# Kernel optimization log

Hardware: AMD Instinct MI355X
Metric: run time of the kernel (lower is better)

## Reference

```python
import jax, jax.numpy as jnp
import numpy as np

BS, LATENT, HID, MAXLEN = 128, 512, 1024, 512

def setup_inputs() -> dict:
    key = jax.random.key(0)
    ks = jax.random.split(key, 12)
    s = 1.0 / np.sqrt(HID)  # pytorch default LSTM init scale
    inp = {}
    inp["decoder_input"] = jax.random.normal(ks[0], (BS, LATENT), jnp.float32)
    inp["lengths"] = jax.random.randint(ks[1], (BS,), 0, MAXLEN)
    # bidirectional single-layer LSTM params (gate order i,f,g,o; combined bias = b_ih+b_hh)
    inp["Wih_f"] = jax.random.uniform(ks[2], (4 * HID, LATENT), jnp.float32, -s, s)
    inp["Whh_f"] = jax.random.uniform(ks[3], (4 * HID, HID), jnp.float32, -s, s)
    inp["b_f"] = jax.random.uniform(ks[4], (4 * HID,), jnp.float32, -s, s)
    inp["Wih_b"] = jax.random.uniform(ks[5], (4 * HID, LATENT), jnp.float32, -s, s)
    inp["Whh_b"] = jax.random.uniform(ks[6], (4 * HID, HID), jnp.float32, -s, s)
    inp["b_b"] = jax.random.uniform(ks[7], (4 * HID,), jnp.float32, -s, s)
    # out: Linear(hidden -> latent); fc1: Linear(2*hidden -> 1)
    inp["W_out"] = jax.random.uniform(ks[8], (LATENT, HID), jnp.float32, -s, s)
    inp["b_out"] = jax.random.uniform(ks[9], (LATENT,), jnp.float32, -s, s)
    inp["W_fc1"] = jax.random.uniform(ks[10], (1, 2 * HID), jnp.float32, -s, s)
    inp["b_fc1"] = jax.random.uniform(ks[11], (1,), jnp.float32, -s, s)
    return inp

def _lstm_cell(x, h, c, Wih, Whh, b):
    z = x @ Wih.T + h @ Whh.T + b  # (bs, 4H)
    i, f, g, o = jnp.split(z, 4, axis=-1)
    c2 = jax.nn.sigmoid(f) * c + jax.nn.sigmoid(i) * jnp.tanh(g)
    h2 = jax.nn.sigmoid(o) * jnp.tanh(c2)
    return h2, c2

def reference(decoder_input, lengths, Wih_f, Whh_f, b_f, Wih_b, Whh_b, b_b,
              W_out, b_out, W_fc1, b_fc1):
    max_len = int(jnp.max(lengths))  # static decode length
    bs = decoder_input.shape[0]
    h0 = jnp.zeros((bs, HID), decoder_input.dtype)

    def step(carry, _):
        x, hf, cf, hb, cb = carry
        # bidirectional LSTM over a length-1 sequence = two cells on same input
        hf, cf = _lstm_cell(x, hf, cf, Wih_f, Whh_f, b_f)
        hb, cb = _lstm_cell(x, hb, cb, Wih_b, Whh_b, b_b)
        out_t = jnp.concatenate([hf, hb], axis=-1)  # (bs, 2H)
        # next input = out(h_n[-1]) i.e. backward-direction hidden
        x_next = hb @ W_out.T + b_out
        return (x_next, hf, cf, hb, cb), out_t

    carry0 = (decoder_input, h0, h0, h0, h0)
    _, outs = jax.lax.scan(step, carry0, xs=None, length=max_len)  # (T, bs, 2H)
    x = jnp.transpose(outs, (1, 0, 2))  # (bs, T, 2H)
    x = jax.nn.relu(x)
    return x @ W_fc1.T + b_fc1  # (bs, T, 1)
```

## Files before the change

### kernel.cpp

```cpp
#include <hip/hip_runtime.h>
#include <math.h>

typedef unsigned short u16;
typedef __attribute__((ext_vector_type(8))) short short8;
typedef __attribute__((ext_vector_type(4))) float f32x4;

__device__ __forceinline__ float sigm(float x) { return 1.0f / (1.0f + expf(-x)); }

__device__ __forceinline__ u16 f2bf(float x) {
    union { float f; unsigned u; } v; v.f = x;
    unsigned r = v.u + 0x7fffu + ((v.u >> 16) & 1u);
    return (u16)(r >> 16);
}
__device__ __forceinline__ float bf2f(u16 h) {
    union { unsigned u; float f; } v; v.u = ((unsigned)h) << 16;
    return v.f;
}
__device__ __forceinline__ f32x4 mfma16(short8 a, short8 b, f32x4 c) {
    return __builtin_amdgcn_mfma_f32_16x16x32_bf16(a, b, c, 0, 0, 0);
}
__device__ __forceinline__ void gl_lds16(const void* g, void* l) {
    __builtin_amdgcn_global_load_lds(
        (const __attribute__((address_space(1))) unsigned int*)g,
        (__attribute__((address_space(3))) unsigned int*)l, 16, 0, 0);
}
__device__ __forceinline__ int swz(int c) { return (c ^ (c >> 2)) & 3; }

#define STAGE_W(kk, buf)                                                      \
    do {                                                                      \
        _Pragma("unroll") for (int i_ = 0; i_ < 2; ++i_)                      \
            gl_lds16(Wsrc + soff[i_] + (kk),                                  \
                     sm + (buf) * 8192 + sldsoff[i_]);                        \
    } while (0)

#define LOAD_A(kk, AH_, AL_)                                                  \
    do {                                                                      \
        _Pragma("unroll") for (int ks_ = 0; ks_ < 2; ++ks_) {                 \
            AH_[ks_] = *(const short8*)(Ah + aoff + (kk) + ks_ * 32);         \
            AL_[ks_] = *(const short8*)(Al + aoff + (kk) + ks_ * 32);         \
        }                                                                     \
    } while (0)

#define COMPUTE(buf, AH_, AL_, cix)                                           \
    do {                                                                      \
        const char* bb_ = sm + (buf) * 8192;                                  \
        _Pragma("unroll") for (int ks_ = 0; ks_ < 2; ++ks_) {                 \
            short8 bh_[2], bl_[2];                                            \
            _Pragma("unroll") for (int nt_ = 0; nt_ < 2; ++nt_) {             \
                const int col_ = nt_ * 16 + l15;                              \
                const int off_ = ks_ * 2048 + col_ * 64 + ((quad ^ swz(col_)) * 16); \
                bh_[nt_] = *(const short8*)(bb_ + off_);                      \
                bl_[nt_] = *(const short8*)(bb_ + 4096 + off_);               \
            }                                                                 \
            _Pragma("unroll") for (int nt_ = 0; nt_ < 2; ++nt_) {             \
                acc[nt_] = mfma16(AH_[ks_], bh_[nt_], acc[nt_]);              \
                acc[nt_] = mfma16(AL_[ks_], bh_[nt_], acc[nt_]);              \
                acc[nt_] = mfma16(AH_[ks_], bl_[nt_], acc[nt_]);              \
            }                                                                 \
        }                                                                     \
        if (fc1w) {                                                           \
            const int kb_ = (cix) * 64 + quad * 8;                            \
            _Pragma("unroll") for (int ks_ = 0; ks_ < 2; ++ks_) {             \
                const float* wp_ = Wfc1 + kb_ + ks_ * 32;                     \
                const f32x4 w0_ = *(const f32x4*)(wp_);                       \
                const f32x4 w1_ = *(const f32x4*)(wp_ + 4);                   \
                const short8 hv_ = AH_[ks_];                                  \
                const short8 lv_ = AL_[ks_];                                  \
                _Pragma("unroll") for (int e_ = 0; e_ < 8; ++e_) {            \
                    const float v_ = bf2f((u16)hv_[e_]) + bf2f((u16)lv_[e_]); \
                    const float wv_ = (e_ < 4) ? w0_[e_] : w1_[e_ - 4];       \
                    fsum = fmaf(fmaxf(v_, 0.0f), wv_, fsum);                  \
                }                                                             \
            }                                                                 \
        }                                                                     \
    } while (0)

__global__ __launch_bounds__(256, 2) void k_step(
    const u16* __restrict__ Ah, const u16* __restrict__ Al,
    u16* __restrict__ NAh, u16* __restrict__ NAl,
    const u16* __restrict__ WH, const u16* __restrict__ WL, int wstride,
    int koff_f, int nch_f, int koff_b, int nch_b,
    const float* __restrict__ BR, float* __restrict__ CF, float* __restrict__ CB,
    const float* __restrict__ Wfc1, const float* __restrict__ bfc1,
    float* __restrict__ out, int T, int t)
{
    __shared__ __align__(16) char sm[16384];

    const int tid = threadIdx.x, bid = blockIdx.x;
    const int w = tid >> 6, lane = tid & 63, l15 = lane & 15, quad = lane >> 4;
    const int dir = bid & 1;
    const int rest = bid >> 1;
    const int rowhalf = rest >> 7, colgrp = rest & 127;
    const int nbase = dir * 4096 + colgrp * 32;
    const int koff = dir ? koff_b : koff_f;
    const int nch  = dir ? nch_b : nch_f;
    const int r0 = rowhalf * 64 + w * 16;

    const bool fc1w = (t > 0) && (dir == 0) && (colgrp == 0);

    const int sp = w >> 1, skh = w & 1;
    const u16* Wsrc = sp ? WL : WH;
    size_t soff[2];
    int sldsoff[2];
#pragma unroll
    for (int i = 0; i < 2; ++i) {
        const int col = i * 16 + (lane >> 2);
        const int s = (lane & 3) ^ swz(col);
        soff[i] = (size_t)(nbase + col) * wstride + (size_t)(koff + skh * 32 + s * 8);
        sldsoff[i] = sp * 4096 + skh * 2048 + i * 1024;
    }

    const size_t aoff = (size_t)(r0 + l15) * 2048 + (size_t)(koff + quad * 8);

    f32x4 acc[2] = {};
    short8 ahA[2], alA[2], ahB[2], alB[2];
    float fsum = 0.0f;

    STAGE_W(0, 0);
    LOAD_A(0, ahA, alA);

    for (int c = 0; c < nch; c += 2) {
        __syncthreads();
        {
            const int k1 = (c + 1) * 64;
            STAGE_W(k1, 1);
            LOAD_A(k1, ahB, alB);
        }
        COMPUTE(0, ahA, alA, c);
        __syncthreads();
        if (c + 2 < nch) {
            const int k2 = (c + 2) * 64;
            STAGE_W(k2, 0);
            LOAD_A(k2, ahA, alA);
        }
        COMPUTE(1, ahB, alB, c + 1);
    }

    __syncthreads();

    if (fc1w) {
        float v = fsum;
        v += __shfl_xor(v, 16);
        v += __shfl_xor(v, 32);
        if (lane < 16) {
            const int m = r0 + l15;
            out[(size_t)m * T + (t - 1)] = v + bfc1[0];
        }
    }

    char* zb = sm + w * 2304;
#pragma unroll
    for (int nt = 0; nt < 2; ++nt)
#pragma unroll
        for (int r = 0; r < 4; ++r)
            *(float*)(zb + (quad * 4 + r) * 144 + (nt * 16 + l15) * 4) = acc[nt][r];
    __syncthreads();

    float* C = dir ? CB : CF;
#pragma unroll
    for (int p2 = 0; p2 < 2; ++p2) {
        const int idx = p2 * 64 + lane;
        const int ml = idx >> 3;
        const int ul = idx & 7;
        const f32x4 z = *(const f32x4*)(zb + ml * 144 + ul * 16);
        const f32x4 b4 = *(const f32x4*)(BR + nbase + ul * 4);
        const float zi = z[0] + b4[0], zf = z[1] + b4[1];
        const float zg = z[2] + b4[2], zo = z[3] + b4[3];
        const int u = colgrp * 8 + ul;
        const int m = r0 + ml;
        const size_t cidx = (size_t)m * 1024 + u;
        const float cold = C[cidx];
        const float c2 = sigm(zf) * cold + sigm(zi) * tanhf(zg);
        const float h2 = sigm(zo) * tanhf(c2);
        C[cidx] = c2;
        const size_t hidx = (size_t)m * 2048 + dir * 1024 + u;
        const u16 hh = f2bf(h2);
        NAh[hidx] = hh;
        NAl[hidx] = f2bf(h2 - bf2f(hh));
    }
}

__global__ __launch_bounds__(256) void k_tail(
    const u16* __restrict__ Ah, const u16* __restrict__ Al,
    const float* __restrict__ Wfc1, const float* __restrict__ bfc1,
    float* __restrict__ out, int T)
{
    __shared__ float red[256];
    const int m = blockIdx.x, tid = threadIdx.x;
    const size_t base = (size_t)m * 2048 + tid * 8;
    const short8 hv = *(const short8*)(Ah + base);
    const short8 lv = *(const short8*)(Al + base);
    float s = 0.0f;
#pragma unroll
    for (int e = 0; e < 8; ++e) {
        const float v = bf2f((u16)hv[e]) + bf2f((u16)lv[e]);
        s = fmaf(fmaxf(v, 0.0f), Wfc1[tid * 8 + e], s);
    }
    red[tid] = s;
    __syncthreads();
    for (int off = 128; off > 0; off >>= 1) {
        if (tid < off) red[tid] += red[tid + off];
        __syncthreads();
    }
    if (tid == 0) out[(size_t)m * T + T - 1] = red[0] + bfc1[0];
}

__global__ __launch_bounds__(256, 1) void k_fold(
    const u16* __restrict__ AH, const u16* __restrict__ AL,
    const u16* __restrict__ BH, const u16* __restrict__ BL,
    const float* __restrict__ Whh_b,
    u16* __restrict__ WH, u16* __restrict__ WL)
{
    const int tid = threadIdx.x, bid = blockIdx.x;
    const int w = tid >> 6, lane = tid & 63, l15 = lane & 15, quad = lane >> 4;
    const int bm = bid >> 4, bn = bid & 15;
    const int ar0 = bm * 64 + (w & 1) * 32;
    const int br0 = bn * 64 + (w >> 1) * 32;
    f32x4 acc[2][2] = {};
    for (int k0 = 0; k0 < 512; k0 += 32) {
        short8 a_h[2], a_l[2], b_h[2], b_l[2];
#pragma unroll
        for (int mt = 0; mt < 2; ++mt) {
            const size_t o = (size_t)(ar0 + mt * 16 + l15) * 512 + k0 + quad * 8;
            a_h[mt] = *(const short8*)(AH + o);
            a_l[mt] = *(const short8*)(AL + o);
        }
#pragma unroll
        for (int nt = 0; nt < 2; ++nt) {
            const size_t o = (size_t)(br0 + nt * 16 + l15) * 512 + k0 + quad * 8;
            b_h[nt] = *(const short8*)(BH + o);
            b_l[nt] = *(const short8*)(BL + o);
        }
#pragma unroll
        for (int mt = 0; mt < 2; ++mt)
#pragma unroll
            for (int nt = 0; nt < 2; ++nt) {
                acc[mt][nt] = mfma16(a_h[mt], b_h[nt], acc[mt][nt]);
                acc[mt][nt] = mfma16(a_l[mt], b_h[nt], acc[mt][nt]);
                acc[mt][nt] = mfma16(a_h[mt], b_l[nt], acc[mt][nt]);
            }
    }
#pragma unroll
    for (int mt = 0; mt < 2; ++mt)
#pragma unroll
        for (int nt = 0; nt < 2; ++nt)
#pragma unroll
            for (int r = 0; r < 4; ++r) {
                const int row = ar0 + mt * 16 + quad * 4 + r;
                const int j = br0 + nt * 16 + l15;
                float v = acc[mt][nt][r];
                if (row >= 4096)
                    v += Whh_b[(size_t)((row & 3) * 1024 + ((row & 4095) >> 2)) * 1024 + j];
                const size_t d = (size_t)row * 2048 + 1024 + j;
                const u16 hh = f2bf(v);
                WH[d] = hh;
                WL[d] = f2bf(v - bf2f(hh));
            }
}

__global__ __launch_bounds__(256) void k_prep(
    const float* __restrict__ dec,
    const float* __restrict__ Wih_f, const float* __restrict__ Whh_f,
    const float* __restrict__ b_f, const float* __restrict__ Wih_b,
    const float* __restrict__ b_b, const float* __restrict__ W_out,
    const float* __restrict__ b_out, const float* __restrict__ b_fc1,
    u16* __restrict__ WihH, u16* __restrict__ WihL,
    u16* __restrict__ WoTH, u16* __restrict__ WoTL,
    float* __restrict__ BR0, float* __restrict__ BR1,
    u16* __restrict__ A0h, u16* __restrict__ A0l,
    u16* __restrict__ WH, u16* __restrict__ WL,
    float* __restrict__ out, int out_size)
{
    const int t = blockIdx.x * 256 + threadIdx.x;
    if (t < 524288) {
        const int colp = t >> 6, kb = (t & 63) * 8;
        const int dir = colp >> 12, u = (colp & 4095) >> 2, g = colp & 3;
        const float* src = (dir ? Wih_b : Wih_f) + (size_t)(g * 1024 + u) * 512 + kb;
        const size_t d = (size_t)colp * 512 + kb;
#pragma unroll
        for (int j = 0; j < 8; ++j) {
            const float v = src[j];
            const u16 hh = f2bf(v);
            WihH[d + j] = hh; WihL[d + j] = f2bf(v - bf2f(hh));
        }
    } else if (t < 589824) {
        const int i = t - 524288, jc = i >> 6, lb = (i & 63) * 8;
#pragma unroll
        for (int jj = 0; jj < 8; ++jj) {
            const float v = W_out[(size_t)(lb + jj) * 1024 + jc];
            const size_t d = (size_t)jc * 512 + lb + jj;
            const u16 hh = f2bf(v);
            WoTH[d] = hh; WoTL[d] = f2bf(v - bf2f(hh));
        }
    } else if (t < 598016) {
        const int colp = t - 589824;
        const int dir = colp >> 12, u = (colp & 4095) >> 2, g = colp & 3;
        const float* Wih = dir ? Wih_b : Wih_f;
        const float s = (dir ? b_b : b_f)[g * 1024 + u];
        BR0[colp] = s;
        float dot = 0.0f;
        for (int l = 0; l < 512; ++l)
            dot += Wih[(size_t)(g * 1024 + u) * 512 + l] * b_out[l];
        BR1[colp] = s + dot;
    } else if (t < 606208) {
        const int i = t - 598016, m = i >> 6, kb = (i & 63) * 8;
#pragma unroll
        for (int j = 0; j < 8; ++j) {
            const float v = dec[(size_t)m * 512 + kb + j];
            const size_t d = (size_t)m * 2048 + kb + j;
            const u16 hh = f2bf(v);
            A0h[d] = hh; A0l[d] = f2bf(v - bf2f(hh));
        }
    } else if (t < 614400) {
        const int base = (t - 606208) * 8;
        const float b0 = b_fc1[0];
#pragma unroll
        for (int j = 0; j < 8; ++j)
            if (base + j < out_size) out[base + j] = b0;
    } else {
        const int i = t - 614400, colp = i >> 7, kb = (i & 127) * 8;
        const int u = colp >> 2, g = colp & 3;
        const float* src = Whh_f + (size_t)(g * 1024 + u) * 1024 + kb;
        const size_t d = (size_t)colp * 2048 + kb;
#pragma unroll
        for (int j = 0; j < 8; ++j) {
            const float v = src[j];
            const u16 hh = f2bf(v);
            WH[d + j] = hh; WL[d + j] = f2bf(v - bf2f(hh));
        }
    }
}

extern "C" void kernel_launch(void* const* d_in, const int* in_sizes, int n_in,
                              void* d_out, int out_size, void* d_ws, size_t ws_size,
                              hipStream_t stream) {
    const float* dec   = (const float*)d_in[0];
    const float* Wih_f = (const float*)d_in[2];
    const float* Whh_f = (const float*)d_in[3];
    const float* b_f   = (const float*)d_in[4];
    const float* Wih_b = (const float*)d_in[5];
    const float* Whh_b = (const float*)d_in[6];
    const float* b_b   = (const float*)d_in[7];
    const float* W_out = (const float*)d_in[8];
    const float* b_out = (const float*)d_in[9];
    const float* W_fc1 = (const float*)d_in[10];
    const float* b_fc1 = (const float*)d_in[11];
    float* out = (float*)d_out;

    char* ws = (char*)d_ws;
    u16* WH    = (u16*)(ws);
    u16* WL    = (u16*)(ws + 33554432);
    u16* WihH  = (u16*)(ws + 67108864);
    u16* WihL  = (u16*)(ws + 75497472);
    u16* WoTH  = (u16*)(ws + 83886080);
    u16* WoTL  = (u16*)(ws + 84934656);
    u16* A0h   = (u16*)(ws + 85983232);
    u16* A0l   = (u16*)(ws + 86507520);
    u16* A1h   = (u16*)(ws + 87031808);
    u16* A1l   = (u16*)(ws + 87556096);
    float* CF  = (float*)(ws + 88080384);
    float* CB  = (float*)(ws + 88604672);
    float* BR0 = (float*)(ws + 89128960);
    float* BR1 = (float*)(ws + 89161728);

    k_prep<<<4448, 256, 0, stream>>>(dec, Wih_f, Whh_f, b_f, Wih_b, b_b,
                                     W_out, b_out, b_fc1,
                                     WihH, WihL, WoTH, WoTL, BR0, BR1,
                                     A0h, A0l, WH, WL, out, out_size);
    k_fold<<<2048, 256, 0, stream>>>(WihH, WihL, WoTH, WoTL, Whh_b, WH, WL);
    hipMemsetAsync(CF, 0, 1048576, stream);

    const int T = out_size / 128;
    u16* Abh[2] = {A0h, A1h};
    u16* Abl[2] = {A0l, A1l};
    for (int t = 0; t < T; ++t) {
        const int in = t & 1, nx = in ^ 1;
        if (t == 0) {
            k_step<<<512, 256, 0, stream>>>(A0h, A0l, A1h, A1l,
                                            WihH, WihL, 512, 0, 8, 0, 8,
                                            BR0, CF, CB, W_fc1, b_fc1, out, T, 0);
        } else {
            k_step<<<512, 256, 0, stream>>>(Abh[in], Abl[in], Abh[nx], Abl[nx],
                                            WH, WL, 2048, 0, 32, 1024, 16,
                                            BR1, CF, CB, W_fc1, b_fc1, out, T, t);
        }
    }
    k_tail<<<128, 256, 0, stream>>>(Abh[T & 1], Abl[T & 1], W_fc1, b_fc1, out, T);
}
```

Measured before the change: 21.80 ms.

## Fuse all LSTM timesteps into one persistent kernel with grid barrier

Replaces the per-timestep k_step launches with a single persistent kernel, k_steps, that loops over all timesteps and synchronises blocks through an atomic-counter grid barrier. Cell state is kept in registers instead of being round-tripped through global CF/CB buffers. The first weight chunk for the next step is prefetched into LDS before the barrier. This removes launch overhead and per-step global traffic, but it depends on all 512 blocks being co-resident (2 per CU on 256 CUs); otherwise the barrier can deadlock, and the spin-wait adds cost of its own.

Result: slower. 43.11 ms (+97.8%).

```diff
diff --git a/kernel.cpp b/kernel.cpp
--- a/kernel.cpp
+++ b/kernel.cpp
@@ -26,11 +26,30 @@
 }
 __device__ __forceinline__ int swz(int c) { return (c ^ (c >> 2)) & 3; }
 
-#define STAGE_W(kk, buf)                                                      \
+__device__ __forceinline__ void grid_barrier(unsigned* cnt, unsigned* gen,
+                                             unsigned nb, unsigned inst) {
+    __syncthreads();
+    if (threadIdx.x == 0) {
+        __threadfence();
+        const unsigned a = __hip_atomic_fetch_add(cnt, 1u, __ATOMIC_ACQ_REL,
+                                                  __HIP_MEMORY_SCOPE_AGENT);
+        if (a == nb * (inst + 1u) - 1u) {
+            __hip_atomic_store(gen, inst + 1u, __ATOMIC_RELEASE,
+                               __HIP_MEMORY_SCOPE_AGENT);
+        } else {
+            while (__hip_atomic_load(gen, __ATOMIC_RELAXED,
+                                     __HIP_MEMORY_SCOPE_AGENT) < inst + 1u)
+                __builtin_amdgcn_s_sleep(2);
+        }
+        __threadfence();
+    }
+    __syncthreads();
+}
+
+#define STAGE2(src, oa, ob, kk, buf)                                          \
     do {                                                                      \
-        _Pragma("unroll") for (int i_ = 0; i_ < 2; ++i_)                      \
-            gl_lds16(Wsrc + soff[i_] + (kk),                                  \
-                     sm + (buf) * 8192 + sldsoff[i_]);                        \
+        gl_lds16((src) + (oa) + (kk), sm + (buf) * 8192 + lds0);              \
+        gl_lds16((src) + (ob) + (kk), sm + (buf) * 8192 + lds1);              \
     } while (0)
 
 #define LOAD_A(kk, AH_, AL_)                                                  \
@@ -75,16 +94,17 @@
         }                                                                     \
     } while (0)
 
-__global__ __launch_bounds__(256, 2) void k_step(
-    const u16* __restrict__ Ah, const u16* __restrict__ Al,
-    u16* __restrict__ NAh, u16* __restrict__ NAl,
-    const u16* __restrict__ WH, const u16* __restrict__ WL, int wstride,
-    int koff_f, int nch_f, int koff_b, int nch_b,
-    const float* __restrict__ BR, float* __restrict__ CF, float* __restrict__ CB,
+__global__ __launch_bounds__(256, 2) void k_steps(
+    u16* A0h, u16* A0l, u16* A1h, u16* A1l,
+    const u16* __restrict__ WihH, const u16* __restrict__ WihL,
+    const u16* __restrict__ WH, const u16* __restrict__ WL,
+    const float* __restrict__ BR0, const float* __restrict__ BR1,
     const float* __restrict__ Wfc1, const float* __restrict__ bfc1,
-    float* __restrict__ out, int T, int t)
+    float* __restrict__ out,
+    unsigned* barcnt, unsigned* bargen, int T)
 {
     __shared__ __align__(16) char sm[16384];
+    __shared__ __align__(16) char ze[9216];
 
     const int tid = threadIdx.x, bid = blockIdx.x;
     const int w = tid >> 6, lane = tid & 63, l15 = lane & 15, quad = lane >> 4;
@@ -92,91 +112,115 @@
     const int rest = bid >> 1;
     const int rowhalf = rest >> 7, colgrp = rest & 127;
     const int nbase = dir * 4096 + colgrp * 32;
-    const int koff = dir ? koff_b : koff_f;
-    const int nch  = dir ? nch_b : nch_f;
     const int r0 = rowhalf * 64 + w * 16;
-
-    const bool fc1w = (t > 0) && (dir == 0) && (colgrp == 0);
+    const bool fc1b = (dir == 0) && (colgrp == 0);
 
     const int sp = w >> 1, skh = w & 1;
-    const u16* Wsrc = sp ? WL : WH;
-    size_t soff[2];
-    int sldsoff[2];
-#pragma unroll
-    for (int i = 0; i < 2; ++i) {
-        const int col = i * 16 + (lane >> 2);
-        const int s = (lane & 3) ^ swz(col);
-        soff[i] = (size_t)(nbase + col) * wstride + (size_t)(koff + skh * 32 + s * 8);
-        sldsoff[i] = sp * 4096 + skh * 2048 + i * 1024;
-    }
-
-    const size_t aoff = (size_t)(r0 + l15) * 2048 + (size_t)(koff + quad * 8);
-
-    f32x4 acc[2] = {};
-    short8 ahA[2], alA[2], ahB[2], alB[2];
-    float fsum = 0.0f;
-
-    STAGE_W(0, 0);
-    LOAD_A(0, ahA, alA);
-
-    for (int c = 0; c < nch; c += 2) {
-        __syncthreads();
-        {
-            const int k1 = (c + 1) * 64;
-            STAGE_W(k1, 1);
-            LOAD_A(k1, ahB, alB);
-        }
-        COMPUTE(0, ahA, alA, c);
-        __syncthreads();
-        if (c + 2 < nch) {
-            const int k2 = (c + 2) * 64;
-            STAGE_W(k2, 0);
-            LOAD_A(k2, ahA, alA);
-        }
-        COMPUTE(1, ahB, alB, c + 1);
-    }
-
-    __syncthreads();
-
-    if (fc1w) {
-        float v = fsum;
-        v += __shfl_xor(v, 16);
-        v += __shfl_xor(v, 32);
-        if (lane < 16) {
-            const int m = r0 + l15;
-            out[(size_t)m * T + (t - 1)] = v + bfc1[0];
-        }
-    }
-
-    char* zb = sm + w * 2304;
-#pragma unroll
-    for (int nt = 0; nt < 2; ++nt)
-#pragma unroll
-        for (int r = 0; r < 4; ++r)
-            *(float*)(zb + (quad * 4 + r) * 144 + (nt * 16 + l15) * 4) = acc[nt][r];
-    __syncthreads();
-
-    float* C = dir ? CB : CF;
-#pragma unroll
-    for (int p2 = 0; p2 < 2; ++p2) {
-        const int idx = p2 * 64 + lane;
-        const int ml = idx >> 3;
-        const int ul = idx & 7;
-        const f32x4 z = *(const f32x4*)(zb + ml * 144 + ul * 16);
-        const f32x4 b4 = *(const f32x4*)(BR + nbase + ul * 4);
-        const float zi = z[0] + b4[0], zf = z[1] + b4[1];
-        const float zg = z[2] + b4[2], zo = z[3] + b4[3];
-        const int u = colgrp * 8 + ul;
-        const int m = r0 + ml;
-        const size_t cidx = (size_t)m * 1024 + u;
-        const float cold = C[cidx];
-        const float c2 = sigm(zf) * cold + sigm(zi) * tanhf(zg);
-        const float h2 = sigm(zo) * tanhf(c2);
-        C[cidx] = c2;
-        const size_t hidx = (size_t)m * 2048 + dir * 1024 + u;
-        const u16 hh = f2bf(h2);
-        NAh[hidx] = hh;
-        NAl[hidx] = f2bf(h2 - bf2f(hh));
+    const u16* Wsrc0 = sp ? WihL : WihH;
+    const u16* WsrcN = sp ? WL : WH;
+    size_t s0a, s0b, sNa, sNb;
+    int lds0, lds1;
+    {
+        const int colA = 0 * 16 + (lane >> 2);
+        const int colB = 1 * 16 + (lane >> 2);
+        const int sa = (lane & 3) ^ swz(colA);
+        const int sb = (lane & 3) ^ swz(colB);
+        const size_t koffN = dir ? 1024 : 0;
+        s0a = (size_t)(nbase + colA) * 512 + (size_t)(skh * 32 + sa * 8);
+        s0b = (size_t)(nbase + colB) * 512 + (size_t)(skh * 32 + sb * 8);
+        sNa = (size_t)(nbase + colA) * 2048 + koffN + (size_t)(skh * 32 + sa * 8);
+        sNb = (size_t)(nbase + colB) * 2048 + koffN + (size_t)(skh * 32 + sb * 8);
+        lds0 = sp * 4096 + skh * 2048;
+        lds1 = lds0 + 1024;
+    }
+
+    const size_t abase = (size_t)(r0 + l15) * 2048 + (size_t)(quad * 8);
+    const size_t aoffN = abase + (size_t)(dir ? 1024 : 0);
+
+    const int ul = lane & 7;
+    const f32x4 br0v = *(const f32x4*)(BR0 + nbase + ul * 4);
+    const f32x4 br1v = *(const f32x4*)(BR1 + nbase + ul * 4);
+    const float b1 = bfc1[0];
+    float creg0 = 0.0f, creg1 = 0.0f;
+
+    const unsigned nb = gridDim.x;
+
+    STAGE2(Wsrc0, s0a, s0b, 0, 0);
+
+    for (int t = 0; t < T; ++t) {
+        const int first = (t == 0);
+        const u16* Ah = (t & 1) ? A1h : A0h;
+        const u16* Al = (t & 1) ? A1l : A0l;
+        u16* NAh = (t & 1) ? A0h : A1h;
+        u16* NAl = (t & 1) ? A0l : A1l;
+        const int nch = first ? 8 : (dir ? 16 : 32);
+        const u16* Wsrc = first ? Wsrc0 : WsrcN;
+        const size_t sA = first ? s0a : sNa;
+        const size_t sB = first ? s0b : sNb;
+        const size_t aoff = first ? abase : aoffN;
+        const bool fc1w = fc1b && (t > 0);
+
+        f32x4 acc[2] = {};
+        short8 ahA[2], alA[2], ahB[2], alB[2];
+        float fsum = 0.0f;
+
+        LOAD_A(0, ahA, alA);
+
+        for (int c = 0; c < nch; c += 2) {
+            __syncthreads();
+            {
+                const int k1 = (c + 1) * 64;
+                STAGE2(Wsrc, sA, sB, k1, 1);
+                LOAD_A(k1, ahB, alB);
+            }
+            COMPUTE(0, ahA, alA, c);
+            __syncthreads();
+            if (c + 2 < nch) {
+                const int k2 = (c + 2) * 64;
+                STAGE2(Wsrc, sA, sB, k2, 0);
+                LOAD_A(k2, ahA, alA);
+            }
+            COMPUTE(1, ahB, alB, c + 1);
+        }
+
+        if (fc1w) {
+            float v = fsum;
+            v += __shfl_xor(v, 16);
+            v += __shfl_xor(v, 32);
+            if (lane < 16)
+                out[(size_t)(r0 + l15) * T + (t - 1)] = v + b1;
+        }
+
+        char* zb = ze + w * 2304;
+#pragma unroll
+        for (int nt = 0; nt < 2; ++nt)
+#pragma unroll
+            for (int r = 0; r < 4; ++r)
+                *(float*)(zb + (quad * 4 + r) * 144 + (nt * 16 + l15) * 4) = acc[nt][r];
+
+        if (t + 1 < T) STAGE2(WsrcN, sNa, sNb, 0, 0);
+
+        const f32x4 bv = first ? br0v : br1v;
+#pragma unroll
+        for (int p2 = 0; p2 < 2; ++p2) {
+            const int ml = p2 * 8 + (lane >> 3);
+            const f32x4 z = *(const f32x4*)(zb + ml * 144 + ul * 16);
+            const float zi = z[0] + bv[0], zf = z[1] + bv[1];
+            const float zg = z[2] + bv[2], zo = z[3] + bv[3];
+            const float cold = p2 ? creg1 : creg0;
+            const float c2 = sigm(zf) * cold + sigm(zi) * tanhf(zg);
+            const float h2 = sigm(zo) * tanhf(c2);
+            if (p2) creg1 = c2; else creg0 = c2;
+            const int u = colgrp * 8 + ul;
+            const int m = r0 + ml;
+            const size_t hidx = (size_t)m * 2048 + dir * 1024 + u;
+            const u16 hh = f2bf(h2);
+            NAh[hidx] = hh;
+            NAl[hidx] = f2bf(h2 - bf2f(hh));
+        }
+
+        if (t + 1 < T)
+            grid_barrier(barcnt, bargen, nb, (unsigned)t);
     }
 }
 
@@ -358,32 +402,23 @@
     u16* A0l   = (u16*)(ws + 86507520);
     u16* A1h   = (u16*)(ws + 87031808);
     u16* A1l   = (u16*)(ws + 87556096);
-    float* CF  = (float*)(ws + 88080384);
-    float* CB  = (float*)(ws + 88604672);
     float* BR0 = (float*)(ws + 89128960);
     float* BR1 = (float*)(ws + 89161728);
+    unsigned* barcnt = (unsigned*)(ws + 89194496);
+    unsigned* bargen = (unsigned*)(ws + 89194624);
 
     k_prep<<<4448, 256, 0, stream>>>(dec, Wih_f, Whh_f, b_f, Wih_b, b_b,
                                      W_out, b_out, b_fc1,
                                      WihH, WihL, WoTH, WoTL, BR0, BR1,
                                      A0h, A0l, WH, WL, out, out_size);
     k_fold<<<2048, 256, 0, stream>>>(WihH, WihL, WoTH, WoTL, Whh_b, WH, WL);
-    hipMemsetAsync(CF, 0, 1048576, stream);
+    hipMemsetAsync(ws + 89194496, 0, 256, stream);
 
     const int T = out_size / 128;
-    u16* Abh[2] = {A0h, A1h};
-    u16* Abl[2] = {A0l, A1l};
-    for (int t = 0; t < T; ++t) {
-        const int in = t & 1, nx = in ^ 1;
-        if (t == 0) {
-            k_step<<<512, 256, 0, stream>>>(A0h, A0l, A1h, A1l,
-                                            WihH, WihL, 512, 0, 8, 0, 8,
-                                            BR0, CF, CB, W_fc1, b_fc1, out, T, 0);
-        } else {
-            k_step<<<512, 256, 0, stream>>>(Abh[in], Abl[in], Abh[nx], Abl[nx],
-                                            WH, WL, 2048, 0, 32, 1024, 16,
-                                            BR1, CF, CB, W_fc1, b_fc1, out, T, t);
-        }
-    }
-    k_tail<<<128, 256, 0, stream>>>(Abh[T & 1], Abl[T & 1], W_fc1, b_fc1, out, T);
-}
+    k_steps<<<512, 256, 0, stream>>>(A0h, A0l, A1h, A1l,
+                                     WihH, WihL, WH, WL,
+                                     BR0, BR1, W_fc1, b_fc1, out,
+                                     barcnt, bargen, T);
+    k_tail<<<128, 256, 0, stream>>>((T & 1) ? A1h : A0h, (T & 1) ? A1l : A0l,
+                                    W_fc1, b_fc1, out, T);
+}
```

## Deepen weight staging to four LDS buffers with vmcnt-gated single barriers

Applied to the files above, without the earlier changes.

Replaces the two-buffer, two-__syncthreads-per-pair loop with a four-stage ring. Each chunk uses one s_barrier, gated by s_waitcnt vmcnt(16), and prefetches both the weight tiles and the A fragments three chunks ahead. The fc1 weights are copied into LDS once, and the gate-staging epilogue gets its own LDS buffer, which removes one block-wide barrier. The goal is to hide global/LDS load latency in the latency-bound per-timestep GEMM. The cost is more LDS and registers, plus a prefetch that runs past the final chunk.

New measurement: 20.79 ms. 4.6% less time.

```diff
diff --git a/kernel.cpp b/kernel.cpp
--- a/kernel.cpp
+++ b/kernel.cpp
@@ -26,11 +26,12 @@
 }
 __device__ __forceinline__ int swz(int c) { return (c ^ (c >> 2)) & 3; }
 
+#define FENCE() asm volatile("" ::: "memory")
+
 #define STAGE_W(kk, buf)                                                      \
     do {                                                                      \
-        _Pragma("unroll") for (int i_ = 0; i_ < 2; ++i_)                      \
-            gl_lds16(Wsrc + soff[i_] + (kk),                                  \
-                     sm + (buf) * 8192 + sldsoff[i_]);                        \
+        gl_lds16(Wsrc + sA + (kk), sm + (buf) * 8192 + lds0);                 \
+        gl_lds16(Wsrc + sB + (kk), sm + (buf) * 8192 + lds1);                 \
     } while (0)
 
 #define LOAD_A(kk, AH_, AL_)                                                  \
@@ -41,9 +42,9 @@
         }                                                                     \
     } while (0)
 
-#define COMPUTE(buf, AH_, AL_, cix)                                           \
+#define COMPUTE(bix, AH_, AL_, cix)                                           \
     do {                                                                      \
-        const char* bb_ = sm + (buf) * 8192;                                  \
+        const char* bb_ = sm + (bix) * 8192;                                  \
         _Pragma("unroll") for (int ks_ = 0; ks_ < 2; ++ks_) {                 \
             short8 bh_[2], bl_[2];                                            \
             _Pragma("unroll") for (int nt_ = 0; nt_ < 2; ++nt_) {             \
@@ -61,7 +62,7 @@
         if (fc1w) {                                                           \
             const int kb_ = (cix) * 64 + quad * 8;                            \
             _Pragma("unroll") for (int ks_ = 0; ks_ < 2; ++ks_) {             \
-                const float* wp_ = Wfc1 + kb_ + ks_ * 32;                     \
+                const float* wp_ = smWf + kb_ + ks_ * 32;                     \
                 const f32x4 w0_ = *(const f32x4*)(wp_);                       \
                 const f32x4 w1_ = *(const f32x4*)(wp_ + 4);                   \
                 const short8 hv_ = AH_[ks_];                                  \
@@ -75,6 +76,17 @@
         }                                                                     \
     } while (0)
 
+#define ITER(cc, BC, BS, AHU, ALU, AHL, ALL)                                  \
+    do {                                                                      \
+        asm volatile("s_waitcnt vmcnt(16)" ::: "memory");                     \
+        __builtin_amdgcn_s_barrier();                                         \
+        FENCE();                                                              \
+        STAGE_W(((cc) + 3) * 64, BS);                                         \
+        FENCE();                                                              \
+        LOAD_A(((cc) + 3) * 64, AHL, ALL);                                    \
+        COMPUTE(BC, AHU, ALU, (cc));                                          \
+    } while (0)
+
 __global__ __launch_bounds__(256, 2) void k_step(
     const u16* __restrict__ Ah, const u16* __restrict__ Al,
     u16* __restrict__ NAh, u16* __restrict__ NAl,
@@ -84,7 +96,9 @@
     const float* __restrict__ Wfc1, const float* __restrict__ bfc1,
     float* __restrict__ out, int T, int t)
 {
-    __shared__ __align__(16) char sm[16384];
+    __shared__ __align__(16) char sm[32768];
+    __shared__ __align__(16) char ze[9216];
+    __shared__ __align__(16) float smWf[2048];
 
     const int tid = threadIdx.x, bid = blockIdx.x;
     const int w = tid >> 6, lane = tid & 63, l15 = lane & 15, quad = lane >> 4;
@@ -96,72 +110,71 @@
     const int nch  = dir ? nch_b : nch_f;
     const int r0 = rowhalf * 64 + w * 16;
 
-    const bool fc1w = (t > 0) && (dir == 0) && (colgrp == 0);
+    const bool fc1b = (dir == 0) && (colgrp == 0);
+    const bool fc1w = fc1b && (t > 0);
 
     const int sp = w >> 1, skh = w & 1;
     const u16* Wsrc = sp ? WL : WH;
-    size_t soff[2];
-    int sldsoff[2];
-#pragma unroll
-    for (int i = 0; i < 2; ++i) {
-        const int col = i * 16 + (lane >> 2);
-        const int s = (lane & 3) ^ swz(col);
-        soff[i] = (size_t)(nbase + col) * wstride + (size_t)(koff + skh * 32 + s * 8);
-        sldsoff[i] = sp * 4096 + skh * 2048 + i * 1024;
+    size_t sA, sB;
+    int lds0, lds1;
+    {
+        const int colA = 0 * 16 + (lane >> 2);
+        const int colB = 1 * 16 + (lane >> 2);
+        const int sa = (lane & 3) ^ swz(colA);
+        const int sb = (lane & 3) ^ swz(colB);
+        sA = (size_t)(nbase + colA) * wstride + (size_t)(koff + skh * 32 + sa * 8);
+        sB = (size_t)(nbase + colB) * wstride + (size_t)(koff + skh * 32 + sb * 8);
+        lds0 = sp * 4096 + skh * 2048;
+        lds1 = lds0 + 1024;
     }
 
     const size_t aoff = (size_t)(r0 + l15) * 2048 + (size_t)(koff + quad * 8);
 
     f32x4 acc[2] = {};
-    short8 ahA[2], alA[2], ahB[2], alB[2];
+    short8 ah0[2], al0[2], ah1[2], al1[2];
+    short8 ah2[2], al2[2], ah3[2], al3[2];
     float fsum = 0.0f;
 
-    STAGE_W(0, 0);
-    LOAD_A(0, ahA, alA);
-
-    for (int c = 0; c < nch; c += 2) {
-        __syncthreads();
-        {
-            const int k1 = (c + 1) * 64;
-            STAGE_W(k1, 1);
-            LOAD_A(k1, ahB, alB);
-        }
-        COMPUTE(0, ahA, alA, c);
-        __syncthreads();
-        if (c + 2 < nch) {
-            const int k2 = (c + 2) * 64;
-            STAGE_W(k2, 0);
-            LOAD_A(k2, ahA, alA);
-        }
-        COMPUTE(1, ahB, alB, c + 1);
-    }
-
-    __syncthreads();
+    if (fc1b) {
+        const f32x4 w0 = *(const f32x4*)(Wfc1 + tid * 8);
+        const f32x4 w1 = *(const f32x4*)(Wfc1 + tid * 8 + 4);
+        *(f32x4*)(smWf + tid * 8) = w0;
+        *(f32x4*)(smWf + tid * 8 + 4) = w1;
+    }
+    asm volatile("s_waitcnt lgkmcnt(0)" ::: "memory");
+
+    STAGE_W(0, 0);   FENCE(); LOAD_A(0, ah0, al0);   FENCE();
+    STAGE_W(64, 1);  FENCE(); LOAD_A(64, ah1, al1);  FENCE();
+    STAGE_W(128, 2); FENCE(); LOAD_A(128, ah2, al2); FENCE();
+
+    for (int c = 0; c < nch; c += 4) {
+        ITER(c + 0, 0, 3, ah0, al0, ah3, al3);
+        ITER(c + 1, 1, 0, ah1, al1, ah0, al0);
+        ITER(c + 2, 2, 1, ah2, al2, ah1, al1);
+        ITER(c + 3, 3, 2, ah3, al3, ah2, al2);
+    }
+    asm volatile("s_waitcnt vmcnt(0)" ::: "memory");
 
     if (fc1w) {
         float v = fsum;
         v += __shfl_xor(v, 16);
         v += __shfl_xor(v, 32);
-        if (lane < 16) {
-            const int m = r0 + l15;
-            out[(size_t)m * T + (t - 1)] = v + bfc1[0];
-        }
-    }
-
-    char* zb = sm + w * 2304;
+        if (lane < 16)
+            out[(size_t)(r0 + l15) * T + (t - 1)] = v + bfc1[0];
+    }
+
+    char* zb = ze + w * 2304;
 #pragma unroll
     for (int nt = 0; nt < 2; ++nt)
 #pragma unroll
         for (int r = 0; r < 4; ++r)
             *(float*)(zb + (quad * 4 + r) * 144 + (nt * 16 + l15) * 4) = acc[nt][r];
-    __syncthreads();
 
     float* C = dir ? CB : CF;
+    const int ul = lane & 7;
 #pragma unroll
     for (int p2 = 0; p2 < 2; ++p2) {
-        const int idx = p2 * 64 + lane;
-        const int ml = idx >> 3;
-        const int ul = idx & 7;
+        const int ml = p2 * 8 + (lane >> 3);
         const f32x4 z = *(const f32x4*)(zb + ml * 144 + ul * 16);
         const f32x4 b4 = *(const f32x4*)(BR + nbase + ul * 4);
         const float zi = z[0] + b4[0], zf = z[1] + b4[1];
```

## Load weight fragments directly from global memory instead of staging through LDS

Applied to the files above, without the earlier changes.

Removes the double-buffered LDS staging of weight tiles (global_load_lds plus block barriers) and has each wave read its bf16 weight fragments straight from global memory into registers for the MFMAs. The epilogue now uses a per-wave LDS region for the accumulator transpose with no block-wide sync. The aim is to cut barrier and LDS traffic in the per-step GEMM. The cost is that each of the four waves in a block loads the same weight columns from global memory, relying on cache to absorb the redundancy, and the explicit prefetch overlap is lost.

Measured after the change: 51.39 ms. +135.8%, slower.

```diff
diff --git a/kernel.cpp b/kernel.cpp
--- a/kernel.cpp
+++ b/kernel.cpp
@@ -19,61 +19,6 @@
 __device__ __forceinline__ f32x4 mfma16(short8 a, short8 b, f32x4 c) {
     return __builtin_amdgcn_mfma_f32_16x16x32_bf16(a, b, c, 0, 0, 0);
 }
-__device__ __forceinline__ void gl_lds16(const void* g, void* l) {
-    __builtin_amdgcn_global_load_lds(
-        (const __attribute__((address_space(1))) unsigned int*)g,
-        (__attribute__((address_space(3))) unsigned int*)l, 16, 0, 0);
-}
-__device__ __forceinline__ int swz(int c) { return (c ^ (c >> 2)) & 3; }
-
-#define STAGE_W(kk, buf)                                                      \
-    do {                                                                      \
-        _Pragma("unroll") for (int i_ = 0; i_ < 2; ++i_)                      \
-            gl_lds16(Wsrc + soff[i_] + (kk),                                  \
-                     sm + (buf) * 8192 + sldsoff[i_]);                        \
-    } while (0)
-
-#define LOAD_A(kk, AH_, AL_)                                                  \
-    do {                                                                      \
-        _Pragma("unroll") for (int ks_ = 0; ks_ < 2; ++ks_) {                 \
-            AH_[ks_] = *(const short8*)(Ah + aoff + (kk) + ks_ * 32);         \
-            AL_[ks_] = *(const short8*)(Al + aoff + (kk) + ks_ * 32);         \
-        }                                                                     \
-    } while (0)
-
-#define COMPUTE(buf, AH_, AL_, cix)                                           \
-    do {                                                                      \
-        const char* bb_ = sm + (buf) * 8192;                                  \
-        _Pragma("unroll") for (int ks_ = 0; ks_ < 2; ++ks_) {                 \
-            short8 bh_[2], bl_[2];                                            \
-            _Pragma("unroll") for (int nt_ = 0; nt_ < 2; ++nt_) {             \
-                const int col_ = nt_ * 16 + l15;                              \
-                const int off_ = ks_ * 2048 + col_ * 64 + ((quad ^ swz(col_)) * 16); \
-                bh_[nt_] = *(const short8*)(bb_ + off_);                      \
-                bl_[nt_] = *(const short8*)(bb_ + 4096 + off_);               \
-            }                                                                 \
-            _Pragma("unroll") for (int nt_ = 0; nt_ < 2; ++nt_) {             \
-                acc[nt_] = mfma16(AH_[ks_], bh_[nt_], acc[nt_]);              \
-                acc[nt_] = mfma16(AL_[ks_], bh_[nt_], acc[nt_]);              \
-                acc[nt_] = mfma16(AH_[ks_], bl_[nt_], acc[nt_]);              \
-            }                                                                 \
-        }                                                                     \
-        if (fc1w) {                                                           \
-            const int kb_ = (cix) * 64 + quad * 8;                            \
-            _Pragma("unroll") for (int ks_ = 0; ks_ < 2; ++ks_) {             \
-                const float* wp_ = Wfc1 + kb_ + ks_ * 32;                     \
-                const f32x4 w0_ = *(const f32x4*)(wp_);                       \
-                const f32x4 w1_ = *(const f32x4*)(wp_ + 4);                   \
-                const short8 hv_ = AH_[ks_];                                  \
-                const short8 lv_ = AL_[ks_];                                  \
-                _Pragma("unroll") for (int e_ = 0; e_ < 8; ++e_) {            \
-                    const float v_ = bf2f((u16)hv_[e_]) + bf2f((u16)lv_[e_]); \
-                    const float wv_ = (e_ < 4) ? w0_[e_] : w1_[e_ - 4];       \
-                    fsum = fmaf(fmaxf(v_, 0.0f), wv_, fsum);                  \
-                }                                                             \
-            }                                                                 \
-        }                                                                     \
-    } while (0)
 
 __global__ __launch_bounds__(256, 2) void k_step(
     const u16* __restrict__ Ah, const u16* __restrict__ Al,
@@ -84,7 +29,7 @@
     const float* __restrict__ Wfc1, const float* __restrict__ bfc1,
     float* __restrict__ out, int T, int t)
 {
-    __shared__ __align__(16) char sm[16384];
+    __shared__ __align__(16) char ze[9216];
 
     const int tid = threadIdx.x, bid = blockIdx.x;
     const int w = tid >> 6, lane = tid & 63, l15 = lane & 15, quad = lane >> 4;
@@ -98,70 +43,69 @@
 
     const bool fc1w = (t > 0) && (dir == 0) && (colgrp == 0);
 
-    const int sp = w >> 1, skh = w & 1;
-    const u16* Wsrc = sp ? WL : WH;
-    size_t soff[2];
-    int sldsoff[2];
-#pragma unroll
-    for (int i = 0; i < 2; ++i) {
-        const int col = i * 16 + (lane >> 2);
-        const int s = (lane & 3) ^ swz(col);
-        soff[i] = (size_t)(nbase + col) * wstride + (size_t)(koff + skh * 32 + s * 8);
-        sldsoff[i] = sp * 4096 + skh * 2048 + i * 1024;
-    }
+    const size_t wq = (size_t)(koff + quad * 8);
+    const u16* WH0 = WH + (size_t)(nbase + l15) * wstride + wq;
+    const u16* WH1 = WH + (size_t)(nbase + 16 + l15) * wstride + wq;
+    const u16* WL0 = WL + (size_t)(nbase + l15) * wstride + wq;
+    const u16* WL1 = WL + (size_t)(nbase + 16 + l15) * wstride + wq;
 
     const size_t aoff = (size_t)(r0 + l15) * 2048 + (size_t)(koff + quad * 8);
 
-    f32x4 acc[2] = {};
-    short8 ahA[2], alA[2], ahB[2], alB[2];
+    f32x4 acc0 = {}, acc1 = {};
     float fsum = 0.0f;
 
-    STAGE_W(0, 0);
-    LOAD_A(0, ahA, alA);
-
-    for (int c = 0; c < nch; c += 2) {
-        __syncthreads();
-        {
-            const int k1 = (c + 1) * 64;
-            STAGE_W(k1, 1);
-            LOAD_A(k1, ahB, alB);
-        }
-        COMPUTE(0, ahA, alA, c);
-        __syncthreads();
-        if (c + 2 < nch) {
-            const int k2 = (c + 2) * 64;
-            STAGE_W(k2, 0);
-            LOAD_A(k2, ahA, alA);
-        }
-        COMPUTE(1, ahB, alB, c + 1);
-    }
-
-    __syncthreads();
+#pragma unroll 2
+    for (int c = 0; c < nch; ++c) {
+        const int kk = c * 64;
+#pragma unroll
+        for (int ks = 0; ks < 2; ++ks) {
+            const int ko = kk + ks * 32;
+            const short8 a_h = *(const short8*)(Ah + aoff + ko);
+            const short8 a_l = *(const short8*)(Al + aoff + ko);
+            const short8 bh0 = *(const short8*)(WH0 + ko);
+            const short8 bh1 = *(const short8*)(WH1 + ko);
+            const short8 bl0 = *(const short8*)(WL0 + ko);
+            const short8 bl1 = *(const short8*)(WL1 + ko);
+            acc0 = mfma16(a_h, bh0, acc0);
+            acc0 = mfma16(a_l, bh0, acc0);
+            acc0 = mfma16(a_h, bl0, acc0);
+            acc1 = mfma16(a_h, bh1, acc1);
+            acc1 = mfma16(a_l, bh1, acc1);
+            acc1 = mfma16(a_h, bl1, acc1);
+            if (fc1w) {
+                const float* wp = Wfc1 + ko + quad * 8;
+                const f32x4 w0 = *(const f32x4*)(wp);
+                const f32x4 w1 = *(const f32x4*)(wp + 4);
+#pragma unroll
+                for (int e = 0; e < 8; ++e) {
+                    const float v = bf2f((u16)a_h[e]) + bf2f((u16)a_l[e]);
+                    const float wv = (e < 4) ? w0[e] : w1[e - 4];
+                    fsum = fmaf(fmaxf(v, 0.0f), wv, fsum);
+                }
+            }
+        }
+    }
 
     if (fc1w) {
         float v = fsum;
         v += __shfl_xor(v, 16);
         v += __shfl_xor(v, 32);
-        if (lane < 16) {
-            const int m = r0 + l15;
-            out[(size_t)m * T + (t - 1)] = v + bfc1[0];
-        }
-    }
-
-    char* zb = sm + w * 2304;
-#pragma unroll
-    for (int nt = 0; nt < 2; ++nt)
-#pragma unroll
-        for (int r = 0; r < 4; ++r)
-            *(float*)(zb + (quad * 4 + r) * 144 + (nt * 16 + l15) * 4) = acc[nt][r];
-    __syncthreads();
+        if (lane < 16)
+            out[(size_t)(r0 + l15) * T + (t - 1)] = v + bfc1[0];
+    }
+
+    char* zb = ze + w * 2304;
+#pragma unroll
+    for (int r = 0; r < 4; ++r) {
+        *(float*)(zb + (quad * 4 + r) * 144 + l15 * 4) = acc0[r];
+        *(float*)(zb + (quad * 4 + r) * 144 + (16 + l15) * 4) = acc1[r];
+    }
 
     float* C = dir ? CB : CF;
+    const int ul = lane & 7;
 #pragma unroll
     for (int p2 = 0; p2 < 2; ++p2) {
-        const int idx = p2 * 64 + lane;
-        const int ml = idx >> 3;
-        const int ul = idx & 7;
+        const int ml = p2 * 8 + (lane >> 3);
         const f32x4 z = *(const f32x4*)(zb + ml * 144 + ul * 16);
         const f32x4 b4 = *(const f32x4*)(BR + nbase + ul * 4);
         const float zi = z[0] + b4[0], zf = z[1] + b4[1];
```
